# Kernel tuning notes

Measured on AMD Instinct MI355X. Metric: run time of the kernel, lower is better.

## Reference

```python
import jax, jax.numpy as jnp
import numpy as np

B, T, D = 16, 4096, 1024
ALPHA0 = 0.4


def setup_inputs() -> dict:
    key = jax.random.key(0)
    k1, k2 = jax.random.split(key)
    input = jax.random.normal(k1, (B, T, D), dtype=jnp.float32)
    hidden = jnp.zeros((B, 1, D), dtype=jnp.float32)
    alpha = jnp.full((1,), ALPHA0, dtype=jnp.float32)
    return {"input": input, "hidden": hidden, "alpha": alpha}


def reference(input, hidden, alpha):
    # EMA linear recurrence: h_t = |a| * x_t + (1 - |a|) * h_{t-1}
    a = jnp.abs(alpha)[0]
    h0 = hidden[:, 0, :]                      # [B, D]
    xs = jnp.swapaxes(input, 0, 1)            # [T, B, D]

    def step(h, x):
        h = a * x + (1.0 - a) * h
        return h, h

    _, ys = jax.lax.scan(step, h0, xs)        # ys: [T, B, D]
    return jnp.swapaxes(ys, 0, 1)             # [B, T, D]
```

## Files before the change

kernel.cpp:

```cpp
#include <hip/hip_runtime.h>


#define B_    16
#define T_    4096
#define D_    1024
#define CHUNK 128
#define WARM  64
#define NC    (T_ / CHUNK)
#define D4    (D_ / 4)

__global__ __launch_bounds__(256) void ema_fused(
    const float* __restrict__ x,
    const float* __restrict__ hidden,
    const float* __restrict__ alpha,
    float* __restrict__ y)
{
    const float a = fabsf(alpha[0]);
    const float f = 1.0f - a;

    const int blk  = blockIdx.x;
    const int b    = blk >> 5;
    const int c    = blk & (NC - 1);
    const int lane = threadIdx.x;

    const int t0 = c * CHUNK;

    float4 h;
    if (c == 0) {
        h = reinterpret_cast<const float4*>(hidden + (size_t)b * D_)[lane];
    } else {
        h = float4{0.f, 0.f, 0.f, 0.f};
        const float4* xw = reinterpret_cast<const float4*>(
            x + ((size_t)b * T_ + (size_t)(t0 - WARM)) * D_) + lane;
#pragma unroll 8
        for (int i = 0; i < WARM; ++i) {
            float4 v = xw[(size_t)i * D4];
            h.x = a * v.x + f * h.x;
            h.y = a * v.y + f * h.y;
            h.z = a * v.z + f * h.z;
            h.w = a * v.w + f * h.w;
        }
    }

    const float4* xv = reinterpret_cast<const float4*>(
        x + ((size_t)b * T_ + (size_t)t0) * D_) + lane;
    float4* yv = reinterpret_cast<float4*>(
        y + ((size_t)b * T_ + (size_t)t0) * D_) + lane;

#pragma unroll 8
    for (int i = 0; i < CHUNK; ++i) {
        float4 v = xv[(size_t)i * D4];
        h.x = a * v.x + f * h.x;
        h.y = a * v.y + f * h.y;
        h.z = a * v.z + f * h.z;
        h.w = a * v.w + f * h.w;
        yv[(size_t)i * D4] = h;
    }
}

extern "C" void kernel_launch(void* const* d_in, const int* in_sizes, int n_in,
                              void* d_out, int out_size, void* d_ws, size_t ws_size,
                              hipStream_t stream) {
    const float* x      = (const float*)d_in[0];
    const float* hidden = (const float*)d_in[1];
    const float* alpha  = (const float*)d_in[2];
    float*       y      = (float*)d_out;

    ema_fused<<<B_ * NC, 256, 0, stream>>>(x, hidden, alpha, y);
}
```

Baseline: 459.6 us.

## Split feature dim across blocks with scalar lanes and nontemporal stores

Each thread now handles one scalar channel instead of a float4, and the D dimension is split into four slices across blocks, giving four times as many blocks for more parallelism and occupancy. Output stores use nontemporal hints so the streamed result does not pollute cache, and launch bounds request higher occupancy. In exchange, memory accesses become 4-byte per lane instead of 16-byte vector loads, and there are more blocks each doing the same warm-up recurrence.

```diff
diff --git a/kernel.cpp b/kernel.cpp
--- a/kernel.cpp
+++ b/kernel.cpp
@@ -7,9 +7,10 @@
 #define CHUNK 128
 #define WARM  64
 #define NC    (T_ / CHUNK)
-#define D4    (D_ / 4)
+#define TPB   256
+#define NSL   (D_ / TPB)
 
-__global__ __launch_bounds__(256) void ema_fused(
+__global__ __launch_bounds__(256, 8) void ema_fused(
     const float* __restrict__ x,
     const float* __restrict__ hidden,
     const float* __restrict__ alpha,
@@ -18,43 +19,33 @@
     const float a = fabsf(alpha[0]);
     const float f = 1.0f - a;
 
-    const int blk  = blockIdx.x;
-    const int b    = blk >> 5;
-    const int c    = blk & (NC - 1);
-    const int lane = threadIdx.x;
+    const int blk = blockIdx.x;
+    const int b   = blk >> 7;
+    const int c   = (blk >> 2) & (NC - 1);
+    const int s   = blk & (NSL - 1);
+    const int d   = s * TPB + threadIdx.x;
 
     const int t0 = c * CHUNK;
+    const float* xcol = x + (size_t)b * T_ * D_ + (size_t)d;
 
-    float4 h;
+    float h;
     if (c == 0) {
-        h = reinterpret_cast<const float4*>(hidden + (size_t)b * D_)[lane];
+        h = hidden[(size_t)b * D_ + d];
     } else {
-        h = float4{0.f, 0.f, 0.f, 0.f};
-        const float4* xw = reinterpret_cast<const float4*>(
-            x + ((size_t)b * T_ + (size_t)(t0 - WARM)) * D_) + lane;
+        h = 0.0f;
+        const float* xw = xcol + (size_t)(t0 - WARM) * D_;
 #pragma unroll 8
-        for (int i = 0; i < WARM; ++i) {
-            float4 v = xw[(size_t)i * D4];
-            h.x = a * v.x + f * h.x;
-            h.y = a * v.y + f * h.y;
-            h.z = a * v.z + f * h.z;
-            h.w = a * v.w + f * h.w;
-        }
+        for (int i = 0; i < WARM; ++i)
+            h = a * xw[(size_t)i * D_] + f * h;
     }
 
-    const float4* xv = reinterpret_cast<const float4*>(
-        x + ((size_t)b * T_ + (size_t)t0) * D_) + lane;
-    float4* yv = reinterpret_cast<float4*>(
-        y + ((size_t)b * T_ + (size_t)t0) * D_) + lane;
+    const float* xv = xcol + (size_t)t0 * D_;
+    float*       yv = y + (size_t)b * T_ * D_ + (size_t)t0 * D_ + (size_t)d;
 
 #pragma unroll 8
     for (int i = 0; i < CHUNK; ++i) {
-        float4 v = xv[(size_t)i * D4];
-        h.x = a * v.x + f * h.x;
-        h.y = a * v.y + f * h.y;
-        h.z = a * v.z + f * h.z;
-        h.w = a * v.w + f * h.w;
-        yv[(size_t)i * D4] = h;
+        h = a * xv[(size_t)i * D_] + f * h;
+        __builtin_nontemporal_store(h, yv + (size_t)i * D_);
     }
 }
 
@@ -66,5 +57,5 @@
     const float* alpha  = (const float*)d_in[2];
     float*       y      = (float*)d_out;
 
-    ema_fused<<<B_ * NC, 256, 0, stream>>>(x, hidden, alpha, y);
+    ema_fused<<<B_ * NC * NSL, TPB, 0, stream>>>(x, hidden, alpha, y);
 }
```

New measurement: 466.0 us. Within noise of the previous version (+1.4%).
